# Performance work log

Hardware: AMD Instinct MI355X
Metric: run time of the kernel (lower is better)

Reference implementation:

```python
import jax, jax.numpy as jnp
import numpy as np
import math

NUM_HEADS = 8
FDIM = 64
NUM_BUCKETS = 32
MAX_DISTANCE = 128


def _relative_position_bucket(rel_pos, num_buckets=NUM_BUCKETS, max_distance=MAX_DISTANCE):
    nb = num_buckets // 2
    ret = (rel_pos >= 0).astype(jnp.int32) * nb
    n = jnp.abs(rel_pos)
    max_exact = nb // 2
    is_small = n < max_exact
    # safe log: clamp n to >=1 where large-branch is unused
    val_large = max_exact + (
        jnp.log(jnp.maximum(n, 1).astype(jnp.float32) / max_exact)
        / math.log(max_distance / max_exact) * (nb - max_exact)
    ).astype(jnp.int32)
    val_large = jnp.minimum(val_large, nb - 1)
    return ret + jnp.where(is_small, n, val_large)


def setup_inputs() -> dict:
    key = jax.random.key(0)
    k = jax.random.split(key, 5)
    B, Nin, F, T = 4, 64, FDIM, 1024
    N = NUM_HEADS * FDIM
    x = jax.random.normal(k[0], (B, Nin, F, T), dtype=jnp.float32)
    # kaiming_normal: std = 1/sqrt(fan_in)
    w_in = jax.random.normal(k[1], (NUM_HEADS, Nin), dtype=jnp.float32) / np.sqrt(Nin)
    w_qk = jax.random.normal(k[2], (2 * N, N), dtype=jnp.float32) / np.sqrt(N)
    w_out = jax.random.normal(k[3], (Nin, NUM_HEADS), dtype=jnp.float32) / np.sqrt(NUM_HEADS)
    rel_bias = jax.random.normal(k[4], (NUM_BUCKETS, NUM_HEADS), dtype=jnp.float32) * 0.02
    return {"x": x, "w_in": w_in, "w_qk": w_qk, "w_out": w_out, "rel_bias": rel_bias}


def reference(x, w_in, w_qk, w_out, rel_bias):
    B, Nin, F, T = x.shape
    h, f = NUM_HEADS, FDIM
    scale = f ** (-0.5)
    # proj_in: 1x1 conv2d Nin -> h
    xi = jnp.einsum('bcft,hc->bhft', x, w_in)          # [B,h,F,T]
    xr = xi.reshape(B, h * f, T)                        # b (h f) t
    v = xr.reshape(B, h, f, T).transpose(0, 1, 3, 2)    # [B,h,T,f]
    # qk: 1x1 conv1d N -> 2N
    qk = jnp.einsum('bct,dc->bdt', xr, w_qk)            # [B,2N,T]
    qk = qk.reshape(B, h, 2 * f, T).transpose(0, 1, 3, 2)  # [B,h,T,2f]
    q, k = qk[..., :f], qk[..., f:]
    sim = jnp.einsum('bhnd,bhmd->bhnm', q, k)           # [B,h,T,T]
    # relative position bias
    q_pos = jnp.arange(T)
    k_pos = jnp.arange(T)
    rel = k_pos[None, :] - q_pos[:, None]               # [T,T]
    buckets = _relative_position_bucket(rel)
    bias = rel_bias[buckets]                            # [T,T,h]
    bias = bias.transpose(2, 0, 1)[None]                # [1,h,T,T]
    sim = (sim + bias) * scale
    attn = jax.nn.softmax(sim, axis=-1)
    out = jnp.einsum('bhnm,bhmd->bhnd', attn, v)        # [B,h,T,f]
    out = out.transpose(0, 1, 3, 2)                     # [B,h,f,T]
    out = jnp.einsum('bhft,ch->bcft', out, w_out)       # [B,Nin,F,T]
    return out
```

## Files before the change

kernel.cpp:

```cpp
#include <hip/hip_runtime.h>
#include <math.h>

#define QSCALE 0.18033688011112042f

typedef __attribute__((ext_vector_type(4))) float  f32x4;
typedef __attribute__((ext_vector_type(2))) float  f32x2;
typedef __attribute__((ext_vector_type(8))) short  bf16x8;
typedef __attribute__((ext_vector_type(4))) short  bf16x4;
typedef __attribute__((ext_vector_type(4))) int    i32x4;

static __device__ __forceinline__ short f2bf(float f) {
    union { float f; unsigned u; } v; v.f = f;
    unsigned r = v.u + 0x7fffu + ((v.u >> 16) & 1u);
    return (short)(r >> 16);
}
static __device__ __forceinline__ int pk2bf(float a, float b) {
    return ((int)f2bf(a) & 0xffff) | ((int)f2bf(b) << 16);
}

#define MFMA16(A,B,C) __builtin_amdgcn_mfma_f32_16x16x32_bf16(A, B, C, 0, 0, 0)

__global__ __launch_bounds__(256) void k_proj_in(
    const float* __restrict__ x, const float* __restrict__ w_in,
    const float* __restrict__ wqk, short* __restrict__ wqk_b,
    short* __restrict__ xi_v, short* __restrict__ xr_t)
{
    __shared__ float w_s[512];
    __shared__ __align__(16) short tr[64 * 72];
    int tid = threadIdx.x;
    int tx = tid & 31, fy = tid >> 5;
    int tb = blockIdx.x, fb = blockIdx.y, b = blockIdx.z;

    {
        int gi = (((b * 8 + fb) * 16 + tb) * 256 + tid) * 4;
        f32x4 wv = *(const f32x4*)&wqk[gi];
        float s = ((gi >> 9) & 64) ? 1.0f : QSCALE;
        bf16x4 pk;
        pk.x = f2bf(wv[0] * s); pk.y = f2bf(wv[1] * s);
        pk.z = f2bf(wv[2] * s); pk.w = f2bf(wv[3] * s);
        *(bf16x4*)&wqk_b[gi] = pk;
    }

    w_s[tid] = w_in[tid & 511];
    w_s[(tid + 256) & 511] = w_in[(tid + 256) & 511];
    __syncthreads();

    int f = fb * 8 + fy;
    int t = tb * 64 + tx * 2;
    float acc[8][2];
    #pragma unroll
    for (int h = 0; h < 8; h++) { acc[h][0] = 0.f; acc[h][1] = 0.f; }

    const float* xp = x + ((size_t)b * 64 * 64 + (size_t)f) * 1024 + t;
    f32x2 buf[8];
    #pragma unroll
    for (int i = 0; i < 8; i++) buf[i] = *(const f32x2*)&xp[(size_t)i * 65536];
    #pragma unroll
    for (int c8 = 0; c8 < 64; c8 += 8) {
        f32x2 cur[8];
        #pragma unroll
        for (int i = 0; i < 8; i++) cur[i] = buf[i];
        if (c8 + 8 < 64) {
            #pragma unroll
            for (int i = 0; i < 8; i++)
                buf[i] = *(const f32x2*)&xp[(size_t)(c8 + 8 + i) * 65536];
        }
        #pragma unroll
        for (int i = 0; i < 8; i++)
            #pragma unroll
            for (int h = 0; h < 8; h++) {
                float wv = w_s[h * 64 + c8 + i];
                acc[h][0] = fmaf(cur[i][0], wv, acc[h][0]);
                acc[h][1] = fmaf(cur[i][1], wv, acc[h][1]);
            }
    }
    #pragma unroll
    for (int h = 0; h < 8; h++)
        *(int*)&xi_v[(((size_t)b * 8 + h) * 64 + f) * 1024 + t] = pk2bf(acc[h][0], acc[h][1]);
    #pragma unroll
    for (int h = 0; h < 8; h++) {
        tr[(tx * 2 + 0) * 72 + h * 8 + fy] = f2bf(acc[h][0]);
        tr[(tx * 2 + 1) * 72 + h * 8 + fy] = f2bf(acc[h][1]);
    }
    __syncthreads();
    int h2 = tid & 7, trow = tid >> 3;
    #pragma unroll
    for (int i = 0; i < 2; i++) {
        int t2 = trow + i * 32;
        i32x4 v = *(const i32x4*)&tr[t2 * 72 + h2 * 8];
        *(i32x4*)&xr_t[((size_t)b * 1024 + tb * 64 + t2) * 512 + h2 * 64 + fb * 8] = v;
    }
}

__global__ __launch_bounds__(256, 4) void k_qk(
    const short* __restrict__ wqk_b, const short* __restrict__ xr_t,
    short* __restrict__ qk_t)
{
    __shared__ __align__(16) short As[64 * 72];
    __shared__ __align__(16) short Bs[64 * 72];
    int tid = threadIdx.x;
    int w = tid >> 6, lane = tid & 63;
    int quad = lane >> 4, l16 = lane & 15;
    int bid = blockIdx.x;
    int wg = (bid & 7) * 128 + (bid >> 3);
    int Dt = wg & 15;
    int tb = (wg >> 4) & 15;
    int b  = wg >> 8;
    int t0 = tb * 64;

    f32x4 acc[4];
    #pragma unroll
    for (int tt = 0; tt < 4; tt++) acc[tt] = (f32x4){0.f,0.f,0.f,0.f};

    int s_row = tid >> 2, s_col = (tid & 3) * 16;
    const short* Ag = wqk_b + ((size_t)Dt * 64 + s_row) * 512;
    const short* Bg = xr_t + ((size_t)b * 1024 + t0 + s_row) * 512;

    i32x4 ga[2], gb[2];
    #pragma unroll
    for (int i = 0; i < 2; i++) {
        ga[i] = *(const i32x4*)&Ag[s_col + i * 8];
        gb[i] = *(const i32x4*)&Bg[s_col + i * 8];
    }

    for (int kk = 0; kk < 512; kk += 64) {
        *(i32x4*)&As[s_row * 72 + s_col]     = ga[0];
        *(i32x4*)&As[s_row * 72 + s_col + 8] = ga[1];
        *(i32x4*)&Bs[s_row * 72 + s_col]     = gb[0];
        *(i32x4*)&Bs[s_row * 72 + s_col + 8] = gb[1];
        __syncthreads();
        if (kk < 448) {
            #pragma unroll
            for (int i = 0; i < 2; i++) {
                ga[i] = *(const i32x4*)&Ag[kk + 64 + s_col + i * 8];
                gb[i] = *(const i32x4*)&Bg[kk + 64 + s_col + i * 8];
            }
        }
        bf16x8 af[2];
        #pragma unroll
        for (int kc = 0; kc < 2; kc++)
            af[kc] = *(const bf16x8*)&As[(w * 16 + l16) * 72 + kc * 32 + quad * 8];
        __builtin_amdgcn_s_setprio(1);
        #pragma unroll
        for (int tt = 0; tt < 4; tt++) {
            bf16x8 bf0 = *(const bf16x8*)&Bs[(tt * 16 + l16) * 72 + quad * 8];
            bf16x8 bf1 = *(const bf16x8*)&Bs[(tt * 16 + l16) * 72 + 32 + quad * 8];
            acc[tt] = MFMA16(af[0], bf0, acc[tt]);
            acc[tt] = MFMA16(af[1], bf1, acc[tt]);
        }
        __builtin_amdgcn_s_setprio(0);
        __syncthreads();
    }
    int h = Dt >> 1;
    int d2 = (Dt & 1) * 64 + w * 16 + quad * 4;
    #pragma unroll
    for (int tt = 0; tt < 4; tt++) {
        bf16x4 pk;
        pk.x = f2bf(acc[tt][0]); pk.y = f2bf(acc[tt][1]);
        pk.z = f2bf(acc[tt][2]); pk.w = f2bf(acc[tt][3]);
        int t = t0 + tt * 16 + l16;
        *(bf16x4*)&qk_t[(((size_t)b * 8 + h) * 1024 + t) * 128 + d2] = pk;
    }
}

__global__ __launch_bounds__(256, 4) void k_attn(
    const short* __restrict__ qk_t, const short* __restrict__ xi_v,
    const float* __restrict__ rel_bias, float* __restrict__ o_part,
    float* __restrict__ lsum)
{
    __shared__ __align__(16) short Ks[64 * 72];
    __shared__ __align__(16) short Vs[64 * 72];
    __shared__ __align__(16) short Ps[4][16 * 72];
    __shared__ float elut[2048];
    int tid = threadIdx.x;
    int w = tid >> 6, lane = tid & 63;
    int quad = lane >> 4, l16 = lane & 15;
    int bid = blockIdx.x;
    int wg = (bid & 7) * 128 + (bid >> 3);
    int nb = wg & 15;
    int mh = (wg >> 4) & 1;
    int bh = wg >> 5;
    int h = bh & 7;
    int n_base = nb * 64;

    for (int i = tid; i < 2047; i += 256) {
        int rel = i - 1023;
        int ret = (rel >= 0) ? 16 : 0;
        int na = rel < 0 ? -rel : rel;
        int idx;
        if (na < 8) idx = ret + na;
        else {
            int vl = 8 + (int)(log2f((float)na * 0.125f) * 2.0f);
            vl = vl > 15 ? 15 : vl;
            idx = ret + vl;
        }
        elut[i] = exp2f(rel_bias[idx * 8 + h] * QSCALE);
    }

    const short* qb = qk_t + (size_t)bh * (1024 * 128);
    const short* vb = xi_v + (size_t)bh * (64 * 1024);

    bf16x8 qf[2];
    #pragma unroll
    for (int kk = 0; kk < 2; kk++)
        qf[kk] = *(const bf16x8*)&qb[(size_t)(n_base + w * 16 + l16) * 128 + kk * 32 + quad * 8];

    f32x4 acc_o[4];
    #pragma unroll
    for (int dt = 0; dt < 4; dt++) acc_o[dt] = (f32x4){0.f,0.f,0.f,0.f};
    float l_st = 0.f;

    int srow = tid >> 2;
    int soff = (tid & 3) * 16;
    int m0 = mh * 512;
    i32x4 gk[2], gv[2];
    #pragma unroll
    for (int i = 0; i < 2; i++) {
        gk[i] = *(const i32x4*)&qb[(size_t)(m0 + srow) * 128 + 64 + soff + i * 8];
        gv[i] = *(const i32x4*)&vb[(size_t)srow * 1024 + m0 + soff + i * 8];
    }

    __syncthreads();

    #pragma unroll 1
    for (int it = 0; it < 8; it++) {
        *(i32x4*)&Ks[srow * 72 + soff]     = gk[0];
        *(i32x4*)&Ks[srow * 72 + soff + 8] = gk[1];
        *(i32x4*)&Vs[srow * 72 + soff]     = gv[0];
        *(i32x4*)&Vs[srow * 72 + soff + 8] = gv[1];
        __syncthreads();
        if (it < 7) {
            int m1 = m0 + 64;
            #pragma unroll
            for (int i = 0; i < 2; i++) {
                gk[i] = *(const i32x4*)&qb[(size_t)(m1 + srow) * 128 + 64 + soff + i * 8];
                gv[i] = *(const i32x4*)&vb[(size_t)srow * 1024 + m1 + soff + i * 8];
            }
        }

        f32x4 s[4];
        __builtin_amdgcn_s_setprio(1);
        #pragma unroll
        for (int mt = 0; mt < 4; mt++) {
            bf16x8 kf0 = *(const bf16x8*)&Ks[(mt * 16 + l16) * 72 + quad * 8];
            bf16x8 kf1 = *(const bf16x8*)&Ks[(mt * 16 + l16) * 72 + 32 + quad * 8];
            f32x4 tacc = (f32x4){0.f,0.f,0.f,0.f};
            tacc = MFMA16(kf0, qf[0], tacc);
            tacc = MFMA16(kf1, qf[1], tacc);
            s[mt] = tacc;
        }
        __builtin_amdgcn_s_setprio(0);

        int n = n_base + w * 16 + l16;
        #pragma unroll
        for (int mt = 0; mt < 4; mt++) {
            int rel0 = m0 + mt * 16 + quad * 4 - n + 1023;
            #pragma unroll
            for (int j = 0; j < 4; j++) {
                float p = exp2f(s[mt][j]) * elut[rel0 + j];
                s[mt][j] = p;
                l_st += p;
            }
        }
        #pragma unroll
        for (int mt = 0; mt < 4; mt++) {
            bf16x4 pk;
            pk.x = f2bf(s[mt][0]); pk.y = f2bf(s[mt][1]);
            pk.z = f2bf(s[mt][2]); pk.w = f2bf(s[mt][3]);
            *(bf16x4*)&Ps[w][l16 * 72 + mt * 16 + quad * 4] = pk;
        }
        __builtin_amdgcn_s_setprio(1);
        #pragma unroll
        for (int si = 0; si < 2; si++) {
            bf16x8 pf = *(const bf16x8*)&Ps[w][l16 * 72 + si * 32 + quad * 8];
            #pragma unroll
            for (int dt = 0; dt < 4; dt++) {
                bf16x8 vf = *(const bf16x8*)&Vs[(dt * 16 + l16) * 72 + si * 32 + quad * 8];
                acc_o[dt] = MFMA16(pf, vf, acc_o[dt]);
            }
        }
        __builtin_amdgcn_s_setprio(0);
        m0 += 64;
        __syncthreads();
    }
    #pragma unroll
    for (int dt = 0; dt < 4; dt++)
        *(f32x4*)&o_part[(((size_t)mh * 32 + bh) * 64 + dt * 16 + l16) * 1024 + n_base + w * 16 + quad * 4] = acc_o[dt];
    l_st += __shfl_xor(l_st, 16);
    l_st += __shfl_xor(l_st, 32);
    if (quad == 0)
        lsum[((size_t)bh * 2 + mh) * 1024 + n_base + w * 16 + l16] = l_st;
}

__global__ __launch_bounds__(512) void k_proj_out(
    const float* __restrict__ o_part, const float* __restrict__ lsum,
    const float* __restrict__ w_out, float* __restrict__ out)
{
    __shared__ float w_s[512];
    __shared__ float o_s[8][64];
    int tid = threadIdx.x;
    int tx = tid & 63, ty = tid >> 6;
    int tb = blockIdx.x, f = blockIdx.y, b = blockIdx.z;
    w_s[tid] = w_out[tid];
    int t = tb * 64 + tx;
    int bh = b * 8 + ty;
    float l0 = lsum[((size_t)bh * 2 + 0) * 1024 + t];
    float l1 = lsum[((size_t)bh * 2 + 1) * 1024 + t];
    float o0 = o_part[((size_t)(0 * 32 + bh) * 64 + f) * 1024 + t];
    float o1 = o_part[((size_t)(1 * 32 + bh) * 64 + f) * 1024 + t];
    o_s[ty][tx] = (o0 + o1) / (l0 + l1);
    __syncthreads();
    float ov[8];
    #pragma unroll
    for (int hh = 0; hh < 8; hh++) ov[hh] = o_s[hh][tx];
    #pragma unroll
    for (int j = 0; j < 8; j++) {
        int c = ty * 8 + j;
        float a = 0.f;
        #pragma unroll
        for (int hh = 0; hh < 8; hh++) a = fmaf(ov[hh], w_s[c * 8 + hh], a);
        out[(((size_t)b * 64 + c) * 64 + f) * 1024 + t] = a;
    }
}

extern "C" void kernel_launch(void* const* d_in, const int* in_sizes, int n_in,
                              void* d_out, int out_size, void* d_ws, size_t ws_size,
                              hipStream_t stream)
{
    const float* x        = (const float*)d_in[0];
    const float* w_in     = (const float*)d_in[1];
    const float* w_qk     = (const float*)d_in[2];
    const float* w_out    = (const float*)d_in[3];
    const float* rel_bias = (const float*)d_in[4];
    float* out = (float*)d_out;

    char* ws = (char*)d_ws;
    short* wqk_b  = (short*)(ws);
    short* xi_v   = (short*)(ws + (size_t)1  * (1 << 20));
    short* xr_t   = (short*)(ws + (size_t)5  * (1 << 20));
    short* qk_t   = (short*)(ws + (size_t)9  * (1 << 20));
    float* o_part = (float*)(ws + (size_t)17 * (1 << 20));
    float* lsum   = (float*)(ws + (size_t)33 * (1 << 20));

    hipLaunchKernelGGL(k_proj_in,  dim3(16, 8, 4),   dim3(256), 0, stream, x, w_in, w_qk, wqk_b, xi_v, xr_t);
    hipLaunchKernelGGL(k_qk,       dim3(1024),       dim3(256), 0, stream, wqk_b, xr_t, qk_t);
    hipLaunchKernelGGL(k_attn,     dim3(1024),       dim3(256), 0, stream, qk_t, xi_v, rel_bias, o_part, lsum);
    hipLaunchKernelGGL(k_proj_out, dim3(16, 64, 4),  dim3(512), 0, stream, o_part, lsum, w_out, out);
}
```

Measured before the change: 160.8 us.

## Fuse four kernels into one persistent kernel with grid-wide atomic barriers

Merges proj_in, qk GEMM, attention and proj_out into a single 1024-block kernel separated by software grid barriers (atomic counter plus spin), removing three kernel launch gaps. The relative-bias exp LUT is built once into global memory by otherwise idle blocks instead of per attention block. proj_out is re-tiled so each block handles 256 timesteps with float4 stores. It depends on all 1024 blocks being co-resident (4 per CU at 256 CUs) and adds a memset plus spin-wait overhead.

Result: slower. 527.4 us (+228.0%).

```diff
diff --git a/kernel.cpp b/kernel.cpp
--- a/kernel.cpp
+++ b/kernel.cpp
@@ -20,306 +20,332 @@
 
 #define MFMA16(A,B,C) __builtin_amdgcn_mfma_f32_16x16x32_bf16(A, B, C, 0, 0, 0)
 
-__global__ __launch_bounds__(256) void k_proj_in(
+static __device__ __forceinline__ void gbar(unsigned* cnt) {
+    __syncthreads();
+    if (threadIdx.x == 0) {
+        __threadfence();
+        atomicAdd(cnt, 1u);
+        while (__hip_atomic_load(cnt, __ATOMIC_RELAXED,
+                                 __HIP_MEMORY_SCOPE_AGENT) < 1024u) {
+            __builtin_amdgcn_s_sleep(2);
+        }
+        __threadfence();
+    }
+    __syncthreads();
+}
+
+__global__ __launch_bounds__(256, 4) void k_fused(
     const float* __restrict__ x, const float* __restrict__ w_in,
-    const float* __restrict__ wqk, short* __restrict__ wqk_b,
-    short* __restrict__ xi_v, short* __restrict__ xr_t)
+    const float* __restrict__ wqk, const float* __restrict__ w_out,
+    const float* __restrict__ rel_bias,
+    short* __restrict__ wqk_b, short* __restrict__ xi_v, short* __restrict__ xr_t,
+    short* __restrict__ qk_t, float* __restrict__ o_part, float* __restrict__ lsum,
+    float* __restrict__ elut_g, unsigned* __restrict__ bar,
+    float* __restrict__ out)
 {
-    __shared__ float w_s[512];
-    __shared__ __align__(16) short tr[64 * 72];
+    __shared__ __align__(16) char smem[36864];
     int tid = threadIdx.x;
-    int tx = tid & 31, fy = tid >> 5;
-    int tb = blockIdx.x, fb = blockIdx.y, b = blockIdx.z;
-
-    {
-        int gi = (((b * 8 + fb) * 16 + tb) * 256 + tid) * 4;
+    int bid = blockIdx.x;
+
+    if (bid < 512) {
+        float* w_s = (float*)smem;
+        short* tr  = (short*)(smem + 2048);
+        int tx = tid & 31, fy = tid >> 5;
+        int tb = bid & 15, fb = (bid >> 4) & 7, b = bid >> 7;
+        w_s[tid] = w_in[tid & 511];
+        w_s[(tid + 256) & 511] = w_in[(tid + 256) & 511];
+        __syncthreads();
+
+        int f = fb * 8 + fy;
+        int t = tb * 64 + tx * 2;
+        float acc[8][2];
+        #pragma unroll
+        for (int h = 0; h < 8; h++) { acc[h][0] = 0.f; acc[h][1] = 0.f; }
+
+        const float* xp = x + ((size_t)b * 64 * 64 + (size_t)f) * 1024 + t;
+        f32x2 buf[8];
+        #pragma unroll
+        for (int i = 0; i < 8; i++) buf[i] = *(const f32x2*)&xp[(size_t)i * 65536];
+        #pragma unroll
+        for (int c8 = 0; c8 < 64; c8 += 8) {
+            f32x2 cur[8];
+            #pragma unroll
+            for (int i = 0; i < 8; i++) cur[i] = buf[i];
+            if (c8 + 8 < 64) {
+                #pragma unroll
+                for (int i = 0; i < 8; i++)
+                    buf[i] = *(const f32x2*)&xp[(size_t)(c8 + 8 + i) * 65536];
+            }
+            #pragma unroll
+            for (int i = 0; i < 8; i++)
+                #pragma unroll
+                for (int h = 0; h < 8; h++) {
+                    float wv = w_s[h * 64 + c8 + i];
+                    acc[h][0] = fmaf(cur[i][0], wv, acc[h][0]);
+                    acc[h][1] = fmaf(cur[i][1], wv, acc[h][1]);
+                }
+        }
+        #pragma unroll
+        for (int h = 0; h < 8; h++)
+            *(int*)&xi_v[(((size_t)b * 8 + h) * 64 + f) * 1024 + t] = pk2bf(acc[h][0], acc[h][1]);
+        #pragma unroll
+        for (int h = 0; h < 8; h++) {
+            tr[(tx * 2 + 0) * 72 + h * 8 + fy] = f2bf(acc[h][0]);
+            tr[(tx * 2 + 1) * 72 + h * 8 + fy] = f2bf(acc[h][1]);
+        }
+        __syncthreads();
+        int h2 = tid & 7, trow = tid >> 3;
+        #pragma unroll
+        for (int i = 0; i < 2; i++) {
+            int t2 = trow + i * 32;
+            i32x4 v = *(const i32x4*)&tr[t2 * 72 + h2 * 8];
+            *(i32x4*)&xr_t[((size_t)b * 1024 + tb * 64 + t2) * 512 + h2 * 64 + fb * 8] = v;
+        }
+    } else {
+        int gi = (((bid - 512) << 8) + tid) << 2;
         f32x4 wv = *(const f32x4*)&wqk[gi];
         float s = ((gi >> 9) & 64) ? 1.0f : QSCALE;
         bf16x4 pk;
         pk.x = f2bf(wv[0] * s); pk.y = f2bf(wv[1] * s);
         pk.z = f2bf(wv[2] * s); pk.w = f2bf(wv[3] * s);
         *(bf16x4*)&wqk_b[gi] = pk;
-    }
-
-    w_s[tid] = w_in[tid & 511];
-    w_s[(tid + 256) & 511] = w_in[(tid + 256) & 511];
-    __syncthreads();
-
-    int f = fb * 8 + fy;
-    int t = tb * 64 + tx * 2;
-    float acc[8][2];
-    #pragma unroll
-    for (int h = 0; h < 8; h++) { acc[h][0] = 0.f; acc[h][1] = 0.f; }
-
-    const float* xp = x + ((size_t)b * 64 * 64 + (size_t)f) * 1024 + t;
-    f32x2 buf[8];
-    #pragma unroll
-    for (int i = 0; i < 8; i++) buf[i] = *(const f32x2*)&xp[(size_t)i * 65536];
-    #pragma unroll
-    for (int c8 = 0; c8 < 64; c8 += 8) {
-        f32x2 cur[8];
-        #pragma unroll
-        for (int i = 0; i < 8; i++) cur[i] = buf[i];
-        if (c8 + 8 < 64) {
-            #pragma unroll
-            for (int i = 0; i < 8; i++)
-                buf[i] = *(const f32x2*)&xp[(size_t)(c8 + 8 + i) * 65536];
-        }
-        #pragma unroll
-        for (int i = 0; i < 8; i++)
-            #pragma unroll
-            for (int h = 0; h < 8; h++) {
-                float wv = w_s[h * 64 + c8 + i];
-                acc[h][0] = fmaf(cur[i][0], wv, acc[h][0]);
-                acc[h][1] = fmaf(cur[i][1], wv, acc[h][1]);
-            }
-    }
-    #pragma unroll
-    for (int h = 0; h < 8; h++)
-        *(int*)&xi_v[(((size_t)b * 8 + h) * 64 + f) * 1024 + t] = pk2bf(acc[h][0], acc[h][1]);
-    #pragma unroll
-    for (int h = 0; h < 8; h++) {
-        tr[(tx * 2 + 0) * 72 + h * 8 + fy] = f2bf(acc[h][0]);
-        tr[(tx * 2 + 1) * 72 + h * 8 + fy] = f2bf(acc[h][1]);
-    }
-    __syncthreads();
-    int h2 = tid & 7, trow = tid >> 3;
-    #pragma unroll
-    for (int i = 0; i < 2; i++) {
-        int t2 = trow + i * 32;
-        i32x4 v = *(const i32x4*)&tr[t2 * 72 + h2 * 8];
-        *(i32x4*)&xr_t[((size_t)b * 1024 + tb * 64 + t2) * 512 + h2 * 64 + fb * 8] = v;
-    }
-}
-
-__global__ __launch_bounds__(256, 4) void k_qk(
-    const short* __restrict__ wqk_b, const short* __restrict__ xr_t,
-    short* __restrict__ qk_t)
-{
-    __shared__ __align__(16) short As[64 * 72];
-    __shared__ __align__(16) short Bs[64 * 72];
-    int tid = threadIdx.x;
-    int w = tid >> 6, lane = tid & 63;
-    int quad = lane >> 4, l16 = lane & 15;
-    int bid = blockIdx.x;
-    int wg = (bid & 7) * 128 + (bid >> 3);
-    int Dt = wg & 15;
-    int tb = (wg >> 4) & 15;
-    int b  = wg >> 8;
-    int t0 = tb * 64;
-
-    f32x4 acc[4];
-    #pragma unroll
-    for (int tt = 0; tt < 4; tt++) acc[tt] = (f32x4){0.f,0.f,0.f,0.f};
-
-    int s_row = tid >> 2, s_col = (tid & 3) * 16;
-    const short* Ag = wqk_b + ((size_t)Dt * 64 + s_row) * 512;
-    const short* Bg = xr_t + ((size_t)b * 1024 + t0 + s_row) * 512;
-
-    i32x4 ga[2], gb[2];
-    #pragma unroll
-    for (int i = 0; i < 2; i++) {
-        ga[i] = *(const i32x4*)&Ag[s_col + i * 8];
-        gb[i] = *(const i32x4*)&Bg[s_col + i * 8];
-    }
-
-    for (int kk = 0; kk < 512; kk += 64) {
-        *(i32x4*)&As[s_row * 72 + s_col]     = ga[0];
-        *(i32x4*)&As[s_row * 72 + s_col + 8] = ga[1];
-        *(i32x4*)&Bs[s_row * 72 + s_col]     = gb[0];
-        *(i32x4*)&Bs[s_row * 72 + s_col + 8] = gb[1];
+        if (tid < 32) {
+            int e = (bid - 512) * 32 + tid;
+            int hh = e >> 11, ii = e & 2047;
+            if (ii < 2047) {
+                int rel = ii - 1023;
+                int ret = (rel >= 0) ? 16 : 0;
+                int na = rel < 0 ? -rel : rel;
+                int idx;
+                if (na < 8) idx = ret + na;
+                else {
+                    int vl = 8 + (int)(log2f((float)na * 0.125f) * 2.0f);
+                    vl = vl > 15 ? 15 : vl;
+                    idx = ret + vl;
+                }
+                elut_g[hh * 2048 + ii] = exp2f(rel_bias[idx * 8 + hh] * QSCALE);
+            }
+        }
+    }
+    gbar(bar + 0);
+
+    {
+        short* As = (short*)smem;
+        short* Bs = (short*)(smem + 9216);
+        int w = tid >> 6, lane = tid & 63;
+        int quad = lane >> 4, l16 = lane & 15;
+        int wg = (bid & 7) * 128 + (bid >> 3);
+        int Dt = wg & 15;
+        int tb = (wg >> 4) & 15;
+        int b  = wg >> 8;
+        int t0 = tb * 64;
+
+        f32x4 acc[4];
+        #pragma unroll
+        for (int tt = 0; tt < 4; tt++) acc[tt] = (f32x4){0.f,0.f,0.f,0.f};
+
+        int s_row = tid >> 2, s_col = (tid & 3) * 16;
+        const short* Ag = wqk_b + ((size_t)Dt * 64 + s_row) * 512;
+        const short* Bg = xr_t + ((size_t)b * 1024 + t0 + s_row) * 512;
+
+        i32x4 ga[2], gb[2];
+        #pragma unroll
+        for (int i = 0; i < 2; i++) {
+            ga[i] = *(const i32x4*)&Ag[s_col + i * 8];
+            gb[i] = *(const i32x4*)&Bg[s_col + i * 8];
+        }
+
+        for (int kk = 0; kk < 512; kk += 64) {
+            *(i32x4*)&As[s_row * 72 + s_col]     = ga[0];
+            *(i32x4*)&As[s_row * 72 + s_col + 8] = ga[1];
+            *(i32x4*)&Bs[s_row * 72 + s_col]     = gb[0];
+            *(i32x4*)&Bs[s_row * 72 + s_col + 8] = gb[1];
+            __syncthreads();
+            if (kk < 448) {
+                #pragma unroll
+                for (int i = 0; i < 2; i++) {
+                    ga[i] = *(const i32x4*)&Ag[kk + 64 + s_col + i * 8];
+                    gb[i] = *(const i32x4*)&Bg[kk + 64 + s_col + i * 8];
+                }
+            }
+            bf16x8 af[2];
+            #pragma unroll
+            for (int kc = 0; kc < 2; kc++)
+                af[kc] = *(const bf16x8*)&As[(w * 16 + l16) * 72 + kc * 32 + quad * 8];
+            __builtin_amdgcn_s_setprio(1);
+            #pragma unroll
+            for (int tt = 0; tt < 4; tt++) {
+                bf16x8 bf0 = *(const bf16x8*)&Bs[(tt * 16 + l16) * 72 + quad * 8];
+                bf16x8 bf1 = *(const bf16x8*)&Bs[(tt * 16 + l16) * 72 + 32 + quad * 8];
+                acc[tt] = MFMA16(af[0], bf0, acc[tt]);
+                acc[tt] = MFMA16(af[1], bf1, acc[tt]);
+            }
+            __builtin_amdgcn_s_setprio(0);
+            __syncthreads();
+        }
+        int h = Dt >> 1;
+        int d2 = (Dt & 1) * 64 + w * 16 + quad * 4;
+        #pragma unroll
+        for (int tt = 0; tt < 4; tt++) {
+            bf16x4 pk;
+            pk.x = f2bf(acc[tt][0]); pk.y = f2bf(acc[tt][1]);
+            pk.z = f2bf(acc[tt][2]); pk.w = f2bf(acc[tt][3]);
+            int t = t0 + tt * 16 + l16;
+            *(bf16x4*)&qk_t[(((size_t)b * 8 + h) * 1024 + t) * 128 + d2] = pk;
+        }
+    }
+    gbar(bar + 1);
+
+    {
+        short* Ks   = (short*)smem;
+        short* Vs   = (short*)(smem + 9216);
+        short* Ps   = (short*)(smem + 18432);
+        float* elut = (float*)(smem + 27648);
+        int w = tid >> 6, lane = tid & 63;
+        int quad = lane >> 4, l16 = lane & 15;
+        int wg = (bid & 7) * 128 + (bid >> 3);
+        int nb = wg & 15;
+        int mh = (wg >> 4) & 1;
+        int bh = wg >> 5;
+        int h = bh & 7;
+        int n_base = nb * 64;
+
+        for (int i = tid; i < 2047; i += 256)
+            elut[i] = elut_g[h * 2048 + i];
+
+        const short* qb = qk_t + (size_t)bh * (1024 * 128);
+        const short* vb = xi_v + (size_t)bh * (64 * 1024);
+
+        bf16x8 qf[2];
+        #pragma unroll
+        for (int kk = 0; kk < 2; kk++)
+            qf[kk] = *(const bf16x8*)&qb[(size_t)(n_base + w * 16 + l16) * 128 + kk * 32 + quad * 8];
+
+        f32x4 acc_o[4];
+        #pragma unroll
+        for (int dt = 0; dt < 4; dt++) acc_o[dt] = (f32x4){0.f,0.f,0.f,0.f};
+        float l_st = 0.f;
+
+        int srow = tid >> 2;
+        int soff = (tid & 3) * 16;
+        int m0 = mh * 512;
+        i32x4 gk[2], gv[2];
+        #pragma unroll
+        for (int i = 0; i < 2; i++) {
+            gk[i] = *(const i32x4*)&qb[(size_t)(m0 + srow) * 128 + 64 + soff + i * 8];
+            gv[i] = *(const i32x4*)&vb[(size_t)srow * 1024 + m0 + soff + i * 8];
+        }
+
         __syncthreads();
-        if (kk < 448) {
-            #pragma unroll
-            for (int i = 0; i < 2; i++) {
-                ga[i] = *(const i32x4*)&Ag[kk + 64 + s_col + i * 8];
-                gb[i] = *(const i32x4*)&Bg[kk + 64 + s_col + i * 8];
-            }
-        }
-        bf16x8 af[2];
-        #pragma unroll
-        for (int kc = 0; kc < 2; kc++)
-            af[kc] = *(const bf16x8*)&As[(w * 16 + l16) * 72 + kc * 32 + quad * 8];
-        __builtin_amdgcn_s_setprio(1);
-        #pragma unroll
-        for (int tt = 0; tt < 4; tt++) {
-            bf16x8 bf0 = *(const bf16x8*)&Bs[(tt * 16 + l16) * 72 + quad * 8];
-            bf16x8 bf1 = *(const bf16x8*)&Bs[(tt * 16 + l16) * 72 + 32 + quad * 8];
-            acc[tt] = MFMA16(af[0], bf0, acc[tt]);
-            acc[tt] = MFMA16(af[1], bf1, acc[tt]);
-        }
-        __builtin_amdgcn_s_setprio(0);
+
+        #pragma unroll 1
+        for (int it = 0; it < 8; it++) {
+            *(i32x4*)&Ks[srow * 72 + soff]     = gk[0];
+            *(i32x4*)&Ks[srow * 72 + soff + 8] = gk[1];
+            *(i32x4*)&Vs[srow * 72 + soff]     = gv[0];
+            *(i32x4*)&Vs[srow * 72 + soff + 8] = gv[1];
+            __syncthreads();
+            if (it < 7) {
+                int m1 = m0 + 64;
+                #pragma unroll
+                for (int i = 0; i < 2; i++) {
+                    gk[i] = *(const i32x4*)&qb[(size_t)(m1 + srow) * 128 + 64 + soff + i * 8];
+                    gv[i] = *(const i32x4*)&vb[(size_t)srow * 1024 + m1 + soff + i * 8];
+                }
+            }
+
+            f32x4 s[4];
+            __builtin_amdgcn_s_setprio(1);
+            #pragma unroll
+            for (int mt = 0; mt < 4; mt++) {
+                bf16x8 kf0 = *(const bf16x8*)&Ks[(mt * 16 + l16) * 72 + quad * 8];
+                bf16x8 kf1 = *(const bf16x8*)&Ks[(mt * 16 + l16) * 72 + 32 + quad * 8];
+                f32x4 tacc = (f32x4){0.f,0.f,0.f,0.f};
+                tacc = MFMA16(kf0, qf[0], tacc);
+                tacc = MFMA16(kf1, qf[1], tacc);
+                s[mt] = tacc;
+            }
+            __builtin_amdgcn_s_setprio(0);
+
+            int n = n_base + w * 16 + l16;
+            #pragma unroll
+            for (int mt = 0; mt < 4; mt++) {
+                int rel0 = m0 + mt * 16 + quad * 4 - n + 1023;
+                #pragma unroll
+                for (int j = 0; j < 4; j++) {
+                    float p = exp2f(s[mt][j]) * elut[rel0 + j];
+                    s[mt][j] = p;
+                    l_st += p;
+                }
+            }
+            #pragma unroll
+            for (int mt = 0; mt < 4; mt++) {
+                bf16x4 pk;
+                pk.x = f2bf(s[mt][0]); pk.y = f2bf(s[mt][1]);
+                pk.z = f2bf(s[mt][2]); pk.w = f2bf(s[mt][3]);
+                *(bf16x4*)&Ps[w * 1152 + l16 * 72 + mt * 16 + quad * 4] = pk;
+            }
+            __builtin_amdgcn_s_setprio(1);
+            #pragma unroll
+            for (int si = 0; si < 2; si++) {
+                bf16x8 pf = *(const bf16x8*)&Ps[w * 1152 + l16 * 72 + si * 32 + quad * 8];
+                #pragma unroll
+                for (int dt = 0; dt < 4; dt++) {
+                    bf16x8 vf = *(const bf16x8*)&Vs[(dt * 16 + l16) * 72 + si * 32 + quad * 8];
+                    acc_o[dt] = MFMA16(pf, vf, acc_o[dt]);
+                }
+            }
+            __builtin_amdgcn_s_setprio(0);
+            m0 += 64;
+            __syncthreads();
+        }
+        #pragma unroll
+        for (int dt = 0; dt < 4; dt++)
+            *(f32x4*)&o_part[(((size_t)mh * 32 + bh) * 64 + dt * 16 + l16) * 1024 + n_base + w * 16 + quad * 4] = acc_o[dt];
+        l_st += __shfl_xor(l_st, 16);
+        l_st += __shfl_xor(l_st, 32);
+        if (quad == 0)
+            lsum[((size_t)bh * 2 + mh) * 1024 + n_base + w * 16 + l16] = l_st;
+    }
+    gbar(bar + 2);
+
+    {
+        float* w_s = (float*)smem;
+        float* o_s = (float*)(smem + 2048);
+        int b = bid >> 8, f = (bid >> 2) & 63, tq = bid & 3;
+        w_s[tid] = w_out[tid & 511];
+        w_s[(tid + 256) & 511] = w_out[(tid + 256) & 511];
+        int t = tq * 256 + tid;
+        #pragma unroll
+        for (int hh = 0; hh < 8; hh++) {
+            int bh = b * 8 + hh;
+            float l0 = lsum[((size_t)bh * 2 + 0) * 1024 + t];
+            float l1 = lsum[((size_t)bh * 2 + 1) * 1024 + t];
+            float o0 = o_part[((size_t)(0 * 32 + bh) * 64 + f) * 1024 + t];
+            float o1 = o_part[((size_t)(1 * 32 + bh) * 64 + f) * 1024 + t];
+            o_s[hh * 256 + tid] = (o0 + o1) / (l0 + l1);
+        }
         __syncthreads();
-    }
-    int h = Dt >> 1;
-    int d2 = (Dt & 1) * 64 + w * 16 + quad * 4;
-    #pragma unroll
-    for (int tt = 0; tt < 4; tt++) {
-        bf16x4 pk;
-        pk.x = f2bf(acc[tt][0]); pk.y = f2bf(acc[tt][1]);
-        pk.z = f2bf(acc[tt][2]); pk.w = f2bf(acc[tt][3]);
-        int t = t0 + tt * 16 + l16;
-        *(bf16x4*)&qk_t[(((size_t)b * 8 + h) * 1024 + t) * 128 + d2] = pk;
-    }
-}
-
-__global__ __launch_bounds__(256, 4) void k_attn(
-    const short* __restrict__ qk_t, const short* __restrict__ xi_v,
-    const float* __restrict__ rel_bias, float* __restrict__ o_part,
-    float* __restrict__ lsum)
-{
-    __shared__ __align__(16) short Ks[64 * 72];
-    __shared__ __align__(16) short Vs[64 * 72];
-    __shared__ __align__(16) short Ps[4][16 * 72];
-    __shared__ float elut[2048];
-    int tid = threadIdx.x;
-    int w = tid >> 6, lane = tid & 63;
-    int quad = lane >> 4, l16 = lane & 15;
-    int bid = blockIdx.x;
-    int wg = (bid & 7) * 128 + (bid >> 3);
-    int nb = wg & 15;
-    int mh = (wg >> 4) & 1;
-    int bh = wg >> 5;
-    int h = bh & 7;
-    int n_base = nb * 64;
-
-    for (int i = tid; i < 2047; i += 256) {
-        int rel = i - 1023;
-        int ret = (rel >= 0) ? 16 : 0;
-        int na = rel < 0 ? -rel : rel;
-        int idx;
-        if (na < 8) idx = ret + na;
-        else {
-            int vl = 8 + (int)(log2f((float)na * 0.125f) * 2.0f);
-            vl = vl > 15 ? 15 : vl;
-            idx = ret + vl;
-        }
-        elut[i] = exp2f(rel_bias[idx * 8 + h] * QSCALE);
-    }
-
-    const short* qb = qk_t + (size_t)bh * (1024 * 128);
-    const short* vb = xi_v + (size_t)bh * (64 * 1024);
-
-    bf16x8 qf[2];
-    #pragma unroll
-    for (int kk = 0; kk < 2; kk++)
-        qf[kk] = *(const bf16x8*)&qb[(size_t)(n_base + w * 16 + l16) * 128 + kk * 32 + quad * 8];
-
-    f32x4 acc_o[4];
-    #pragma unroll
-    for (int dt = 0; dt < 4; dt++) acc_o[dt] = (f32x4){0.f,0.f,0.f,0.f};
-    float l_st = 0.f;
-
-    int srow = tid >> 2;
-    int soff = (tid & 3) * 16;
-    int m0 = mh * 512;
-    i32x4 gk[2], gv[2];
-    #pragma unroll
-    for (int i = 0; i < 2; i++) {
-        gk[i] = *(const i32x4*)&qb[(size_t)(m0 + srow) * 128 + 64 + soff + i * 8];
-        gv[i] = *(const i32x4*)&vb[(size_t)srow * 1024 + m0 + soff + i * 8];
-    }
-
-    __syncthreads();
-
-    #pragma unroll 1
-    for (int it = 0; it < 8; it++) {
-        *(i32x4*)&Ks[srow * 72 + soff]     = gk[0];
-        *(i32x4*)&Ks[srow * 72 + soff + 8] = gk[1];
-        *(i32x4*)&Vs[srow * 72 + soff]     = gv[0];
-        *(i32x4*)&Vs[srow * 72 + soff + 8] = gv[1];
-        __syncthreads();
-        if (it < 7) {
-            int m1 = m0 + 64;
-            #pragma unroll
-            for (int i = 0; i < 2; i++) {
-                gk[i] = *(const i32x4*)&qb[(size_t)(m1 + srow) * 128 + 64 + soff + i * 8];
-                gv[i] = *(const i32x4*)&vb[(size_t)srow * 1024 + m1 + soff + i * 8];
-            }
-        }
-
-        f32x4 s[4];
-        __builtin_amdgcn_s_setprio(1);
-        #pragma unroll
-        for (int mt = 0; mt < 4; mt++) {
-            bf16x8 kf0 = *(const bf16x8*)&Ks[(mt * 16 + l16) * 72 + quad * 8];
-            bf16x8 kf1 = *(const bf16x8*)&Ks[(mt * 16 + l16) * 72 + 32 + quad * 8];
-            f32x4 tacc = (f32x4){0.f,0.f,0.f,0.f};
-            tacc = MFMA16(kf0, qf[0], tacc);
-            tacc = MFMA16(kf1, qf[1], tacc);
-            s[mt] = tacc;
-        }
-        __builtin_amdgcn_s_setprio(0);
-
-        int n = n_base + w * 16 + l16;
-        #pragma unroll
-        for (int mt = 0; mt < 4; mt++) {
-            int rel0 = m0 + mt * 16 + quad * 4 - n + 1023;
-            #pragma unroll
-            for (int j = 0; j < 4; j++) {
-                float p = exp2f(s[mt][j]) * elut[rel0 + j];
-                s[mt][j] = p;
-                l_st += p;
-            }
-        }
-        #pragma unroll
-        for (int mt = 0; mt < 4; mt++) {
-            bf16x4 pk;
-            pk.x = f2bf(s[mt][0]); pk.y = f2bf(s[mt][1]);
-            pk.z = f2bf(s[mt][2]); pk.w = f2bf(s[mt][3]);
-            *(bf16x4*)&Ps[w][l16 * 72 + mt * 16 + quad * 4] = pk;
-        }
-        __builtin_amdgcn_s_setprio(1);
-        #pragma unroll
-        for (int si = 0; si < 2; si++) {
-            bf16x8 pf = *(const bf16x8*)&Ps[w][l16 * 72 + si * 32 + quad * 8];
-            #pragma unroll
-            for (int dt = 0; dt < 4; dt++) {
-                bf16x8 vf = *(const bf16x8*)&Vs[(dt * 16 + l16) * 72 + si * 32 + quad * 8];
-                acc_o[dt] = MFMA16(pf, vf, acc_o[dt]);
-            }
-        }
-        __builtin_amdgcn_s_setprio(0);
-        m0 += 64;
-        __syncthreads();
-    }
-    #pragma unroll
-    for (int dt = 0; dt < 4; dt++)
-        *(f32x4*)&o_part[(((size_t)mh * 32 + bh) * 64 + dt * 16 + l16) * 1024 + n_base + w * 16 + quad * 4] = acc_o[dt];
-    l_st += __shfl_xor(l_st, 16);
-    l_st += __shfl_xor(l_st, 32);
-    if (quad == 0)
-        lsum[((size_t)bh * 2 + mh) * 1024 + n_base + w * 16 + l16] = l_st;
-}
-
-__global__ __launch_bounds__(512) void k_proj_out(
-    const float* __restrict__ o_part, const float* __restrict__ lsum,
-    const float* __restrict__ w_out, float* __restrict__ out)
-{
-    __shared__ float w_s[512];
-    __shared__ float o_s[8][64];
-    int tid = threadIdx.x;
-    int tx = tid & 63, ty = tid >> 6;
-    int tb = blockIdx.x, f = blockIdx.y, b = blockIdx.z;
-    w_s[tid] = w_out[tid];
-    int t = tb * 64 + tx;
-    int bh = b * 8 + ty;
-    float l0 = lsum[((size_t)bh * 2 + 0) * 1024 + t];
-    float l1 = lsum[((size_t)bh * 2 + 1) * 1024 + t];
-    float o0 = o_part[((size_t)(0 * 32 + bh) * 64 + f) * 1024 + t];
-    float o1 = o_part[((size_t)(1 * 32 + bh) * 64 + f) * 1024 + t];
-    o_s[ty][tx] = (o0 + o1) / (l0 + l1);
-    __syncthreads();
-    float ov[8];
-    #pragma unroll
-    for (int hh = 0; hh < 8; hh++) ov[hh] = o_s[hh][tx];
-    #pragma unroll
-    for (int j = 0; j < 8; j++) {
-        int c = ty * 8 + j;
-        float a = 0.f;
-        #pragma unroll
-        for (int hh = 0; hh < 8; hh++) a = fmaf(ov[hh], w_s[c * 8 + hh], a);
-        out[(((size_t)b * 64 + c) * 64 + f) * 1024 + t] = a;
+        int tx4 = tid & 63, ty2 = tid >> 6;
+        f32x4 ov[8];
+        #pragma unroll
+        for (int hh = 0; hh < 8; hh++)
+            ov[hh] = *(const f32x4*)&o_s[hh * 256 + tx4 * 4];
+        size_t obase = ((size_t)b * 64 * 64 + f) * 1024 + tq * 256 + tx4 * 4;
+        #pragma unroll
+        for (int j = 0; j < 16; j++) {
+            int c = ty2 * 16 + j;
+            f32x4 a = (f32x4){0.f,0.f,0.f,0.f};
+            #pragma unroll
+            for (int hh = 0; hh < 8; hh++) {
+                float wv = w_s[c * 8 + hh];
+                a[0] = fmaf(ov[hh][0], wv, a[0]);
+                a[1] = fmaf(ov[hh][1], wv, a[1]);
+                a[2] = fmaf(ov[hh][2], wv, a[2]);
+                a[3] = fmaf(ov[hh][3], wv, a[3]);
+            }
+            *(f32x4*)&out[obase + (size_t)c * 65536] = a;
+        }
     }
 }
 
@@ -329,7 +355,7 @@
 {
     const float* x        = (const float*)d_in[0];
     const float* w_in     = (const float*)d_in[1];
-    const float* w_qk     = (const float*)d_in[2];
+    const float* wqk      = (const float*)d_in[2];
     const float* w_out    = (const float*)d_in[3];
     const float* rel_bias = (const float*)d_in[4];
     float* out = (float*)d_out;
@@ -341,9 +367,13 @@
     short* qk_t   = (short*)(ws + (size_t)9  * (1 << 20));
     float* o_part = (float*)(ws + (size_t)17 * (1 << 20));
     float* lsum   = (float*)(ws + (size_t)33 * (1 << 20));
-
-    hipLaunchKernelGGL(k_proj_in,  dim3(16, 8, 4),   dim3(256), 0, stream, x, w_in, w_qk, wqk_b, xi_v, xr_t);
-    hipLaunchKernelGGL(k_qk,       dim3(1024),       dim3(256), 0, stream, wqk_b, xr_t, qk_t);
-    hipLaunchKernelGGL(k_attn,     dim3(1024),       dim3(256), 0, stream, qk_t, xi_v, rel_bias, o_part, lsum);
-    hipLaunchKernelGGL(k_proj_out, dim3(16, 64, 4),  dim3(512), 0, stream, o_part, lsum, w_out, out);
-}
+    float* elut_g = (float*)(ws + (size_t)33 * (1 << 20) + 262144);
+    unsigned* bar = (unsigned*)(ws + (size_t)33 * (1 << 20) + 524288);
+
+    hipMemsetAsync(bar, 0, 64, stream);
+
+    hipLaunchKernelGGL(k_fused, dim3(1024), dim3(256), 0, stream,
+                       x, w_in, wqk, w_out, rel_bias,
+                       wqk_b, xi_v, xr_t, qk_t, o_part, lsum,
+                       elut_g, bar, out);
+}
```

## Precompute bias exp LUT once, store attention partials as bf16, vectorize proj_out

Applied to the files above, without the earlier changes.

The per-head exp(bias) lookup table is now computed once in k_proj_in into global memory, instead of being recomputed with log2/exp2 by every attention block. Attention partial outputs are written as bf16 rather than fp32, which halves their write and read traffic. k_proj_out is restructured so each thread covers 4 timesteps with float4 stores and reuses loaded head values across 16 output channels. The cost is lower precision in the partial sums and an extra global table read per attention block.

Result: no change. 157.7 us (median of 2 runs) (-2.0%).

```diff
diff --git a/kernel.cpp b/kernel.cpp
--- a/kernel.cpp
+++ b/kernel.cpp
@@ -14,6 +14,10 @@
     unsigned r = v.u + 0x7fffu + ((v.u >> 16) & 1u);
     return (short)(r >> 16);
 }
+static __device__ __forceinline__ float bf2f(short s) {
+    union { unsigned u; float f; } v; v.u = ((unsigned)(unsigned short)s) << 16;
+    return v.f;
+}
 static __device__ __forceinline__ int pk2bf(float a, float b) {
     return ((int)f2bf(a) & 0xffff) | ((int)f2bf(b) << 16);
 }
@@ -22,7 +26,8 @@
 
 __global__ __launch_bounds__(256) void k_proj_in(
     const float* __restrict__ x, const float* __restrict__ w_in,
-    const float* __restrict__ wqk, short* __restrict__ wqk_b,
+    const float* __restrict__ wqk, const float* __restrict__ rel_bias,
+    short* __restrict__ wqk_b, float* __restrict__ elut_g,
     short* __restrict__ xi_v, short* __restrict__ xr_t)
 {
     __shared__ float w_s[512];
@@ -30,15 +35,33 @@
     int tid = threadIdx.x;
     int tx = tid & 31, fy = tid >> 5;
     int tb = blockIdx.x, fb = blockIdx.y, b = blockIdx.z;
+    int bflat = (b * 8 + fb) * 16 + tb;
 
     {
-        int gi = (((b * 8 + fb) * 16 + tb) * 256 + tid) * 4;
+        int gi = (bflat * 256 + tid) * 4;
         f32x4 wv = *(const f32x4*)&wqk[gi];
         float s = ((gi >> 9) & 64) ? 1.0f : QSCALE;
         bf16x4 pk;
         pk.x = f2bf(wv[0] * s); pk.y = f2bf(wv[1] * s);
         pk.z = f2bf(wv[2] * s); pk.w = f2bf(wv[3] * s);
         *(bf16x4*)&wqk_b[gi] = pk;
+    }
+    if (bflat < 64) {
+        int e = bflat * 256 + tid;
+        int hh = e >> 11, ii = e & 2047;
+        if (ii < 2047) {
+            int rel = ii - 1023;
+            int ret = (rel >= 0) ? 16 : 0;
+            int na = rel < 0 ? -rel : rel;
+            int idx;
+            if (na < 8) idx = ret + na;
+            else {
+                int vl = 8 + (int)(log2f((float)na * 0.125f) * 2.0f);
+                vl = vl > 15 ? 15 : vl;
+                idx = ret + vl;
+            }
+            elut_g[hh * 2048 + ii] = exp2f(rel_bias[idx * 8 + hh] * QSCALE);
+        }
     }
 
     w_s[tid] = w_in[tid & 511];
@@ -165,7 +188,7 @@
 
 __global__ __launch_bounds__(256, 4) void k_attn(
     const short* __restrict__ qk_t, const short* __restrict__ xi_v,
-    const float* __restrict__ rel_bias, float* __restrict__ o_part,
+    const float* __restrict__ elut_g, short* __restrict__ o_part,
     float* __restrict__ lsum)
 {
     __shared__ __align__(16) short Ks[64 * 72];
@@ -183,19 +206,8 @@
     int h = bh & 7;
     int n_base = nb * 64;
 
-    for (int i = tid; i < 2047; i += 256) {
-        int rel = i - 1023;
-        int ret = (rel >= 0) ? 16 : 0;
-        int na = rel < 0 ? -rel : rel;
-        int idx;
-        if (na < 8) idx = ret + na;
-        else {
-            int vl = 8 + (int)(log2f((float)na * 0.125f) * 2.0f);
-            vl = vl > 15 ? 15 : vl;
-            idx = ret + vl;
-        }
-        elut[i] = exp2f(rel_bias[idx * 8 + h] * QSCALE);
-    }
+    for (int i = tid; i < 2047; i += 256)
+        elut[i] = elut_g[h * 2048 + i];
 
     const short* qb = qk_t + (size_t)bh * (1024 * 128);
     const short* vb = xi_v + (size_t)bh * (64 * 1024);
@@ -284,42 +296,58 @@
         __syncthreads();
     }
     #pragma unroll
-    for (int dt = 0; dt < 4; dt++)
-        *(f32x4*)&o_part[(((size_t)mh * 32 + bh) * 64 + dt * 16 + l16) * 1024 + n_base + w * 16 + quad * 4] = acc_o[dt];
+    for (int dt = 0; dt < 4; dt++) {
+        bf16x4 pk;
+        pk.x = f2bf(acc_o[dt][0]); pk.y = f2bf(acc_o[dt][1]);
+        pk.z = f2bf(acc_o[dt][2]); pk.w = f2bf(acc_o[dt][3]);
+        *(bf16x4*)&o_part[(((size_t)mh * 32 + bh) * 64 + dt * 16 + l16) * 1024 + n_base + w * 16 + quad * 4] = pk;
+    }
     l_st += __shfl_xor(l_st, 16);
     l_st += __shfl_xor(l_st, 32);
     if (quad == 0)
         lsum[((size_t)bh * 2 + mh) * 1024 + n_base + w * 16 + l16] = l_st;
 }
 
-__global__ __launch_bounds__(512) void k_proj_out(
-    const float* __restrict__ o_part, const float* __restrict__ lsum,
+__global__ __launch_bounds__(256) void k_proj_out(
+    const short* __restrict__ o_part, const float* __restrict__ lsum,
     const float* __restrict__ w_out, float* __restrict__ out)
 {
     __shared__ float w_s[512];
-    __shared__ float o_s[8][64];
+    __shared__ float o_s[8][256];
     int tid = threadIdx.x;
-    int tx = tid & 63, ty = tid >> 6;
-    int tb = blockIdx.x, f = blockIdx.y, b = blockIdx.z;
+    int tq = blockIdx.x, f = blockIdx.y, b = blockIdx.z;
     w_s[tid] = w_out[tid];
-    int t = tb * 64 + tx;
-    int bh = b * 8 + ty;
-    float l0 = lsum[((size_t)bh * 2 + 0) * 1024 + t];
-    float l1 = lsum[((size_t)bh * 2 + 1) * 1024 + t];
-    float o0 = o_part[((size_t)(0 * 32 + bh) * 64 + f) * 1024 + t];
-    float o1 = o_part[((size_t)(1 * 32 + bh) * 64 + f) * 1024 + t];
-    o_s[ty][tx] = (o0 + o1) / (l0 + l1);
+    w_s[tid + 256] = w_out[tid + 256];
+    int t = tq * 256 + tid;
+    #pragma unroll
+    for (int hh = 0; hh < 8; hh++) {
+        int bh = b * 8 + hh;
+        float l0 = lsum[((size_t)bh * 2 + 0) * 1024 + t];
+        float l1 = lsum[((size_t)bh * 2 + 1) * 1024 + t];
+        float o0 = bf2f(o_part[((size_t)(0 * 32 + bh) * 64 + f) * 1024 + t]);
+        float o1 = bf2f(o_part[((size_t)(1 * 32 + bh) * 64 + f) * 1024 + t]);
+        o_s[hh][tid] = (o0 + o1) / (l0 + l1);
+    }
     __syncthreads();
-    float ov[8];
-    #pragma unroll
-    for (int hh = 0; hh < 8; hh++) ov[hh] = o_s[hh][tx];
-    #pragma unroll
-    for (int j = 0; j < 8; j++) {
-        int c = ty * 8 + j;
-        float a = 0.f;
-        #pragma unroll
-        for (int hh = 0; hh < 8; hh++) a = fmaf(ov[hh], w_s[c * 8 + hh], a);
-        out[(((size_t)b * 64 + c) * 64 + f) * 1024 + t] = a;
+    int tx4 = tid & 63, ty2 = tid >> 6;
+    f32x4 ov[8];
+    #pragma unroll
+    for (int hh = 0; hh < 8; hh++)
+        ov[hh] = *(const f32x4*)&o_s[hh][tx4 * 4];
+    size_t obase = ((size_t)b * 64 * 64 + f) * 1024 + tq * 256 + tx4 * 4;
+    #pragma unroll
+    for (int j = 0; j < 16; j++) {
+        int c = ty2 * 16 + j;
+        f32x4 a = (f32x4){0.f,0.f,0.f,0.f};
+        #pragma unroll
+        for (int hh = 0; hh < 8; hh++) {
+            float wv = w_s[c * 8 + hh];
+            a[0] = fmaf(ov[hh][0], wv, a[0]);
+            a[1] = fmaf(ov[hh][1], wv, a[1]);
+            a[2] = fmaf(ov[hh][2], wv, a[2]);
+            a[3] = fmaf(ov[hh][3], wv, a[3]);
+        }
+        *(f32x4*)&out[obase + (size_t)c * 65536] = a;
     }
 }
 
@@ -329,7 +357,7 @@
 {
     const float* x        = (const float*)d_in[0];
     const float* w_in     = (const float*)d_in[1];
-    const float* w_qk     = (const float*)d_in[2];
+    const float* wqk      = (const float*)d_in[2];
     const float* w_out    = (const float*)d_in[3];
     const float* rel_bias = (const float*)d_in[4];
     float* out = (float*)d_out;
@@ -339,11 +367,13 @@
     short* xi_v   = (short*)(ws + (size_t)1  * (1 << 20));
     short* xr_t   = (short*)(ws + (size_t)5  * (1 << 20));
     short* qk_t   = (short*)(ws + (size_t)9  * (1 << 20));
-    float* o_part = (float*)(ws + (size_t)17 * (1 << 20));
-    float* lsum   = (float*)(ws + (size_t)33 * (1 << 20));
-
-    hipLaunchKernelGGL(k_proj_in,  dim3(16, 8, 4),   dim3(256), 0, stream, x, w_in, w_qk, wqk_b, xi_v, xr_t);
-    hipLaunchKernelGGL(k_qk,       dim3(1024),       dim3(256), 0, stream, wqk_b, xr_t, qk_t);
-    hipLaunchKernelGGL(k_attn,     dim3(1024),       dim3(256), 0, stream, qk_t, xi_v, rel_bias, o_part, lsum);
-    hipLaunchKernelGGL(k_proj_out, dim3(16, 64, 4),  dim3(512), 0, stream, o_part, lsum, w_out, out);
-}
+    short* o_part = (short*)(ws + (size_t)17 * (1 << 20));
+    float* lsum   = (float*)(ws + (size_t)25 * (1 << 20));
+    float* elut_g = (float*)(ws + (size_t)25 * (1 << 20) + 262144);
+
+    hipLaunchKernelGGL(k_proj_in,  dim3(16, 8, 4), dim3(256), 0, stream,
+                       x, w_in, wqk, rel_bias, wqk_b, elut_g, xi_v, xr_t);
+    hipLaunchKernelGGL(k_qk,       dim3(1024),     dim3(256), 0, stream, wqk_b, xr_t, qk_t);
+    hipLaunchKernelGGL(k_attn,     dim3(1024),     dim3(256), 0, stream, qk_t, xi_v, elut_g, o_part, lsum);
+    hipLaunchKernelGGL(k_proj_out, dim3(4, 64, 4), dim3(256), 0, stream, o_part, lsum, w_out, out);
+}
```
